# Kernel tuning notes

Measured on AMD Instinct MI355X. Metric: run time of the kernel, lower is better.

## Reference

```python
import jax, jax.numpy as jnp
import numpy as np

V, E, H, T, B = 33278, 400, 1150, 128, 32
LAYER_DIMS = [(E, H), (H, H), (H, E)]  # (input, hidden) per layer; last tied -> E


def _uniform(key, shape, scale):
    return jax.random.uniform(key, shape, jnp.float32, -scale, scale)


def setup_inputs() -> dict:
    key = jax.random.key(0)
    ks = jax.random.split(key, 20)
    inp = {
        'input': jax.random.randint(ks[0], (T, B), 0, V),
        'emb_W': _uniform(ks[1], (V, E), 0.1),
        'final_b': jnp.zeros((V,), jnp.float32),
    }
    ki = 2
    for l, (din, dh) in enumerate(LAYER_DIMS):
        s = 1.0 / np.sqrt(dh)
        inp[f'Wih_l{l}'] = _uniform(ks[ki + 0], (4 * dh, din), s)
        inp[f'Whh_l{l}'] = _uniform(ks[ki + 1], (4 * dh, dh), s)
        inp[f'bih_l{l}'] = _uniform(ks[ki + 2], (4 * dh,), s)
        inp[f'bhh_l{l}'] = _uniform(ks[ki + 3], (4 * dh,), s)
        ki += 4
        inp[f'h0_l{l}'] = jnp.zeros((B, dh), jnp.float32)
        inp[f'c0_l{l}'] = jnp.zeros((B, dh), jnp.float32)
    return inp


def lstm_layer(x, h0, c0, Wih, Whh, bih, bhh):
    # x: [T, B, din]; PyTorch gate order i, f, g, o
    xg = jnp.einsum('tbi,gi->tbg', x, Wih) + bih  # [T, B, 4H]

    def step(carry, xg_t):
        h, c = carry
        g = xg_t + h @ Whh.T + bhh
        i, f, gg, o = jnp.split(g, 4, axis=-1)
        c = jax.nn.sigmoid(f) * c + jax.nn.sigmoid(i) * jnp.tanh(gg)
        h = jax.nn.sigmoid(o) * jnp.tanh(c)
        return (h, c), h

    (hT, cT), ys = jax.lax.scan(step, (h0, c0), xg)
    return ys, hT, cT


def reference(input, emb_W, final_b,
              Wih_l0, Whh_l0, bih_l0, bhh_l0,
              Wih_l1, Whh_l1, bih_l1, bhh_l1,
              Wih_l2, Whh_l2, bih_l2, bhh_l2,
              h0_l0, c0_l0, h0_l1, c0_l1, h0_l2, c0_l2):
    # Eval-mode AWD-LSTM encoder: all dropouts are identity.
    x = emb_W[input]  # [T, B, E]
    params = [(Wih_l0, Whh_l0, bih_l0, bhh_l0, h0_l0, c0_l0),
              (Wih_l1, Whh_l1, bih_l1, bhh_l1, h0_l1, c0_l1),
              (Wih_l2, Whh_l2, bih_l2, bhh_l2, h0_l2, c0_l2)]
    new_hidden = []
    for (Wih, Whh, bih, bhh, h0, c0) in params:
        x, hT, cT = lstm_layer(x, h0, c0, Wih, Whh, bih, bhh)
        new_hidden.extend([hT, cT])
    # Tied decoder: final.weight = embedding.weight ([V, E])
    logits = jnp.einsum('tbe,ve->tbv', x, emb_W) + final_b  # [T, B, V]
    return (logits, *new_hidden)
```

## Files before the change

### kernel.cpp

```cpp
#include <hip/hip_runtime.h>
#include <math.h>

#define T_ 128
#define B_ 32
#define V_ 33278
#define E_ 400

typedef __bf16 bf16x8 __attribute__((ext_vector_type(8)));
typedef float f32x4 __attribute__((ext_vector_type(4)));

#define AGENT_LD(p) __hip_atomic_load((p), __ATOMIC_RELAXED, __HIP_MEMORY_SCOPE_AGENT)
#define AGENT_ST(p, v) __hip_atomic_store((p), (v), __ATOMIC_RELAXED, __HIP_MEMORY_SCOPE_AGENT)

__device__ __forceinline__ float exp2f_(float x) {
  float r;
  asm("v_exp_f32 %0, %1" : "=v"(r) : "v"(x));
  return r;
}
__device__ __forceinline__ float rcpf_(float x) {
  float r;
  asm("v_rcp_f32 %0, %1" : "=v"(r) : "v"(x));
  return r;
}
__device__ __forceinline__ float sigf_(float x) { return rcpf_(1.0f + exp2f_(-1.44269504f * x)); }
__device__ __forceinline__ float tanhf_(float x) {
  float t = exp2f_(2.88539008f * x);
  return 1.0f - 2.0f * rcpf_(t + 1.0f);
}

__device__ __forceinline__ unsigned short f2bf(float f) {
  unsigned u = __float_as_uint(f);
  unsigned lsb = (u >> 16) & 1;
  return (unsigned short)((u + 0x7FFFu + lsb) >> 16);
}

__device__ __forceinline__ void gload16(const unsigned short* g, unsigned short* l) {
  __builtin_amdgcn_global_load_lds((const __attribute__((address_space(1))) void*)g,
                                   (__attribute__((address_space(3))) void*)l, 16, 0, 0);
}

__global__ void embed_kernel(const int* __restrict__ idx, const float* __restrict__ W,
                             unsigned short* __restrict__ x) {
  int i = blockIdx.x * blockDim.x + threadIdx.x;
  if (i >= T_ * B_ * 416) return;
  int k = i % 416;
  int tb = i / 416;
  x[i] = (k < E_) ? f2bf(W[(size_t)idx[tb] * E_ + k]) : 0;
}

__global__ void convW(const float* __restrict__ in, unsigned short* __restrict__ out, int N, int K,
                      int Kp, long total) {
  long i = (long)blockIdx.x * blockDim.x + threadIdx.x;
  if (i >= total) return;
  int k = (int)(i % Kp);
  long n = i / Kp;
  out[i] = (n < N && k < K) ? f2bf(in[n * (long)K + k]) : 0;
}

__global__ __launch_bounds__(256) void gemm_bf16(const unsigned short* __restrict__ A,
                                                 const unsigned short* __restrict__ B,
                                                 const float* __restrict__ bias0,
                                                 const float* __restrict__ bias1,
                                                 float* __restrict__ C, int M, int Kp, int ldc,
                                                 int realN, int gateN) {
  __shared__ __align__(16) unsigned short lsA[4 * 128 * 8];
  __shared__ __align__(16) unsigned short lsB[4 * 128 * 8];
  const int tid = threadIdx.x;
  const int lane = tid & 63;
  const int w = tid >> 6;
  const int wm = (w >> 1) * 64;
  const int wn = (w & 1) * 64;
  const int lr = lane & 15;
  const int kq = lane >> 4;
  const int m0 = blockIdx.y * 128;
  const int n0 = blockIdx.x * 128;

  f32x4 acc[4][4] = {};

  const int kiters = Kp >> 5;
  for (int kt = 0; kt < kiters; ++kt) {
    const int k0 = kt << 5;
#pragma unroll
    for (int q = 0; q < 2; ++q) {
      int s = w + q * 4;
      int kc = s >> 1, rb = (s & 1) * 64;
      gload16(A + (size_t)(m0 + rb + lane) * Kp + k0 + kc * 8, lsA + s * 512);
      gload16(B + (size_t)(n0 + rb + lane) * Kp + k0 + kc * 8, lsB + s * 512);
    }
    __syncthreads();

    bf16x8 af[4], bf[4];
#pragma unroll
    for (int mf = 0; mf < 4; ++mf)
      af[mf] = *(const bf16x8*)&lsA[(kq * 128 + wm + mf * 16 + lr) * 8];
#pragma unroll
    for (int nf = 0; nf < 4; ++nf)
      bf[nf] = *(const bf16x8*)&lsB[(kq * 128 + wn + nf * 16 + lr) * 8];
#pragma unroll
    for (int mf = 0; mf < 4; ++mf)
#pragma unroll
      for (int nf = 0; nf < 4; ++nf)
        acc[mf][nf] = __builtin_amdgcn_mfma_f32_16x16x32_bf16(af[mf], bf[nf], acc[mf][nf], 0, 0, 0);
    __syncthreads();
  }

#pragma unroll
  for (int nf = 0; nf < 4; ++nf) {
    int n = n0 + wn + nf * 16 + lr;
    if (n >= realN) continue;
    float bsum = 0.0f;
    if (bias0) bsum += bias0[n];
    if (bias1) bsum += bias1[n];
    int col = n;
    if (gateN > 0) {
      int g = (n >= gateN) + (n >= 2 * gateN) + (n >= 3 * gateN);
      int u = n - g * gateN;
      col = u * 4 + g;
    }
#pragma unroll
    for (int mf = 0; mf < 4; ++mf) {
      int mbase = m0 + wm + mf * 16 + kq * 4;
#pragma unroll
      for (int r = 0; r < 4; ++r) C[(size_t)(mbase + r) * ldc + col] = acc[mf][nf][r] + bsum;
    }
  }
}


struct FP {
  float* xg;
  const unsigned short *whh0, *wih1, *whh1, *wih2, *whh2;
  const float *h0_0, *c0_0, *h0_1, *c0_1, *h0_2, *c0_2;
  const float *bih1, *bhh1, *bih2, *bhh2;
  unsigned short *xc1, *xc2, *xc3;
  float *oh0, *oc0, *oh1, *oc1, *oh2, *oc2;
  int* flags;
};

__device__ __forceinline__ void pollset(const int* f, int hf, int n, int tgt) {
  int lane = threadIdx.x & 63;
  for (;;) {
    int v = (lane < n) ? AGENT_LD(&f[((lane << 1) + hf) * 16]) : tgt;
    if (__all(v >= tgt)) break;
  }
}

__device__ __forceinline__ void pollone(const int* f, int tgt) {
  for (;;) {
    int v = AGENT_LD(f);
    if (__all(v >= tgt)) break;
  }
}

template <int KT>
__device__ __forceinline__ void stage(const unsigned short* slab, unsigned short* lds) {
  constexpr int KP = KT * 32, KPP = KP + 8, C16 = KP / 8, NCH = 16 * C16;
  constexpr int NIT = (NCH + 511) / 512;
  const int tid = threadIdx.x;
  uint4 d[NIT];
#pragma unroll
  for (int i = 0; i < NIT; ++i) {
    int c = tid + i * 512;
    if (c < NCH) d[i] = *(const uint4*)(slab + (size_t)(c / C16) * KP + (c % C16) * 8);
  }
#pragma unroll
  for (int i = 0; i < NIT; ++i) {
    int c = tid + i * 512;
    if (c < NCH) *(uint4*)&lds[(c / C16) * KPP + (c % C16) * 8] = d[i];
  }
}

template <int KTA, int KTB>
__device__ __forceinline__ void stage2(const unsigned short* slabA, const unsigned short* slabB,
                                       unsigned short* ldsA, unsigned short* ldsB) {
  constexpr int KPA = KTA * 32, KPPA = KPA + 8, CA = KPA / 8, NA = 16 * CA;
  constexpr int NITA = (NA + 511) / 512;
  constexpr int KPB = KTB * 32, KPPB = KPB + 8, CB = KPB / 8, NB = 16 * CB;
  constexpr int NITB = (NB + 511) / 512;
  const int tid = threadIdx.x;
  uint4 dA[NITA], dB[NITB];
#pragma unroll
  for (int i = 0; i < NITA; ++i) {
    int c = tid + i * 512;
    if (c < NA) dA[i] = *(const uint4*)(slabA + (size_t)(c / CA) * KPA + (c % CA) * 8);
  }
#pragma unroll
  for (int i = 0; i < NITB; ++i) {
    int c = tid + i * 512;
    if (c < NB) dB[i] = *(const uint4*)(slabB + (size_t)(c / CB) * KPB + (c % CB) * 8);
  }
#pragma unroll
  for (int i = 0; i < NITA; ++i) {
    int c = tid + i * 512;
    if (c < NA) *(uint4*)&ldsA[(c / CA) * KPPA + (c % CA) * 8] = dA[i];
  }
#pragma unroll
  for (int i = 0; i < NITB; ++i) {
    int c = tid + i * 512;
    if (c < NB) *(uint4*)&ldsB[(c / CB) * KPPB + (c % CB) * 8] = dB[i];
  }
}

template <int KT>
__device__ __forceinline__ void load_aw(const unsigned short* w, int dh, int U0, int wv, int lm,
                                        int kq, bf16x8* aw) {
  const int ga = lm & 3, ula = lm >> 2;
  const int ua = U0 + wv * 4 + ula;
  const unsigned short* wr = w + (size_t)(ga * dh + (ua < dh ? ua : 0)) * (KT * 32);
#pragma unroll
  for (int kt = 0; kt < KT; ++kt) aw[kt] = *(const bf16x8*)&wr[kt * 32 + kq * 8];
}

template <int KT>
__device__ __forceinline__ void mm4(const bf16x8* aw, const unsigned short* lds, int lm, int kq,
                                    f32x4& a0, f32x4& a1, f32x4& a2, f32x4& a3) {
  constexpr int KPP = KT * 32 + 8;
  const unsigned short* rp = lds + lm * KPP + kq * 8;
#pragma unroll
  for (int kt = 0; kt < KT; kt += 4) {
    a0 = __builtin_amdgcn_mfma_f32_16x16x32_bf16(aw[kt], *(const bf16x8*)&rp[kt * 32], a0, 0, 0, 0);
    if (kt + 1 < KT)
      a1 = __builtin_amdgcn_mfma_f32_16x16x32_bf16(aw[kt + 1], *(const bf16x8*)&rp[(kt + 1) * 32],
                                                   a1, 0, 0, 0);
    if (kt + 2 < KT)
      a2 = __builtin_amdgcn_mfma_f32_16x16x32_bf16(aw[kt + 2], *(const bf16x8*)&rp[(kt + 2) * 32],
                                                   a2, 0, 0, 0);
    if (kt + 3 < KT)
      a3 = __builtin_amdgcn_mfma_f32_16x16x32_bf16(aw[kt + 3], *(const bf16x8*)&rp[(kt + 3) * 32],
                                                   a3, 0, 0, 0);
  }
}

__device__ __forceinline__ void pub_h(unsigned short* dst, float hn, bool vu, int kq) {
  unsigned hv = vu ? (unsigned)f2bf(hn) : 0u;
  unsigned t16 = (unsigned)__shfl_xor((int)hv, 16);
  unsigned v32 = (kq & 1) ? (t16 | (hv << 16)) : (hv | (t16 << 16));
  unsigned o32 = (unsigned)__shfl_xor((int)v32, 32);
  if (kq == 0)
    AGENT_ST((unsigned long long*)dst, (unsigned long long)v32 | ((unsigned long long)o32 << 32));
}

__global__ __launch_bounds__(512, 2) void fused_lstm(FP P) {
  __shared__ __align__(16) unsigned short sbuf[16 * 1160 + 16 * 424];
  const int tid = threadIdx.x;
  const int lane = tid & 63;
  const int wv = tid >> 6;
  const int lm = lane & 15;
  const int kq = lane >> 4;
  const int bid = blockIdx.x;
  int* f0 = P.flags;
  int* fh = P.flags + 72 * 16;
  int* f1 = P.flags + 144 * 16;
  int* f2 = P.flags + 216 * 16;
  int* agg = P.flags + 4096;

  if (bid >= 242) {
    if (wv != 0) return;
    const int aset = bid - 242;
    const int hf = aset & 1;
    const int* fset = (aset < 2) ? f0 : f1;
    int* aline = &agg[aset * 16];
    for (int k = 1; k <= T_ + 1; ++k) {
      for (;;) {
        int v = (lane < 36) ? AGENT_LD(&fset[((lane << 1) + hf) * 16]) : k;
        if (__all(v >= k)) break;
      }
      if (lane == 0) AGENT_ST(aline, k);
    }
    return;
  }

  if (bid < 72) {
    constexpr int KT = 36, KP = 1152;
    const int hf = bid & 1, gid = bid >> 1, U0 = gid * 32;
    const int gb = hf * 16 + lm, un = U0 + wv * 4 + kq;
    const bool vu = un < 1150;
    bf16x8 aw[KT];
    load_aw<KT>(P.whh0, 1150, U0, wv, lm, kq, aw);
    float creg = vu ? P.c0_0[gb * 1150 + un] : 0.f;
    pub_h(P.xc1 + (size_t)gb * KP + U0 + wv * 4, vu ? P.h0_0[gb * 1150 + un] : 0.f, vu, kq);
    asm volatile("s_waitcnt vmcnt(0)" ::: "memory");
    __syncthreads();
    if (tid == 0) AGENT_ST(&f0[(gid * 2 + hf) * 16], 1);
    for (int t = 0; t < T_; ++t) {
      f32x4 cinit = *(const f32x4*)&P.xg[(size_t)(t * 32 + gb) * 4608 + un * 4];
      if (wv == 0) pollone(&agg[hf * 16], t + 1);
      __syncthreads();
      stage<KT>(P.xc1 + (size_t)(t * 32 + hf * 16) * KP, sbuf);
      __syncthreads();
      f32x4 a0 = cinit, a1 = {0.f, 0.f, 0.f, 0.f}, a2 = {0.f, 0.f, 0.f, 0.f},
            a3 = {0.f, 0.f, 0.f, 0.f};
      mm4<KT>(aw, sbuf, lm, kq, a0, a1, a2, a3);
      float gi = a0[0] + a1[0] + a2[0] + a3[0], gf = a0[1] + a1[1] + a2[1] + a3[1];
      float gg = a0[2] + a1[2] + a2[2] + a3[2], go = a0[3] + a1[3] + a2[3] + a3[3];
      float cn = sigf_(gf) * creg + sigf_(gi) * tanhf_(gg);
      float hn = sigf_(go) * tanhf_(cn);
      creg = cn;
      pub_h(P.xc1 + (size_t)((t + 1) * 32 + gb) * KP + U0 + wv * 4, hn, vu, kq);
      if (t == T_ - 1 && vu) { P.oh0[gb * 1150 + un] = hn; P.oc0[gb * 1150 + un] = cn; }
      asm volatile("s_waitcnt vmcnt(0)" ::: "memory");
      __syncthreads();
      if (tid == 0) AGENT_ST(&f0[(gid * 2 + hf) * 16], t + 2);
    }
  } else if (bid < 144) {
    constexpr int KT = 36, KP = 1152;
    const int idx = bid - 72, hf = idx & 1, gid = idx >> 1, U0 = gid * 32;
    const int gb = hf * 16 + lm, un = U0 + wv * 4 + kq;
    const bool vu = un < 1150;
    bf16x8 aw[KT];
    load_aw<KT>(P.wih1, 1150, U0, wv, lm, kq, aw);
    f32x4 bini = {0.f, 0.f, 0.f, 0.f};
    if (vu) {
#pragma unroll
      for (int g = 0; g < 4; ++g) bini[g] = P.bih1[g * 1150 + un] + P.bhh1[g * 1150 + un];
    }
    for (int t = 0; t < T_; ++t) {
      if (wv == 0) pollone(&agg[hf * 16], t + 2);
      __syncthreads();
      stage<KT>(P.xc1 + (size_t)((t + 1) * 32 + hf * 16) * KP, sbuf);
      __syncthreads();
      f32x4 a0 = bini, a1 = {0.f, 0.f, 0.f, 0.f}, a2 = {0.f, 0.f, 0.f, 0.f},
            a3 = {0.f, 0.f, 0.f, 0.f};
      mm4<KT>(aw, sbuf, lm, kq, a0, a1, a2, a3);
      float r0 = a0[0] + a1[0] + a2[0] + a3[0], r1 = a0[1] + a1[1] + a2[1] + a3[1];
      float r2 = a0[2] + a1[2] + a2[2] + a3[2], r3 = a0[3] + a1[3] + a2[3] + a3[3];
      unsigned long long* dst =
          (unsigned long long*)(P.xg + (size_t)(t * 32 + gb) * 4608 + un * 4);
      AGENT_ST(dst, ((unsigned long long)__float_as_uint(r1) << 32) | __float_as_uint(r0));
      AGENT_ST(dst + 1, ((unsigned long long)__float_as_uint(r3) << 32) | __float_as_uint(r2));
      asm volatile("s_waitcnt vmcnt(0)" ::: "memory");
      __syncthreads();
      if (tid == 0) AGENT_ST(&fh[(gid * 2 + hf) * 16], t + 1);
    }
  } else if (bid < 216) {
    constexpr int KT = 36, KP = 1152;
    const int idx = bid - 144, hf = idx & 1, gid = idx >> 1, U0 = gid * 32;
    const int gb = hf * 16 + lm, un = U0 + wv * 4 + kq;
    const bool vu = un < 1150;
    bf16x8 aw[KT];
    load_aw<KT>(P.whh1, 1150, U0, wv, lm, kq, aw);
    float creg = vu ? P.c0_1[gb * 1150 + un] : 0.f;
    pub_h(P.xc2 + (size_t)gb * KP + U0 + wv * 4, vu ? P.h0_1[gb * 1150 + un] : 0.f, vu, kq);
    asm volatile("s_waitcnt vmcnt(0)" ::: "memory");
    __syncthreads();
    if (tid == 0) AGENT_ST(&f1[(gid * 2 + hf) * 16], 1);
    for (int t = 0; t < T_; ++t) {
      if (wv == 0) pollone(&agg[32 + hf * 16], t + 1);
      else if (wv == 1) pollone(&fh[(gid * 2 + hf) * 16], t + 1);
      __syncthreads();
      stage<KT>(P.xc2 + (size_t)(t * 32 + hf * 16) * KP, sbuf);
      const unsigned long long* rp =
          (const unsigned long long*)(P.xg + (size_t)(t * 32 + gb) * 4608 + un * 4);
      unsigned long long q0 = AGENT_LD(rp), q1 = AGENT_LD(rp + 1);
      __syncthreads();
      f32x4 a0, a1 = {0.f, 0.f, 0.f, 0.f}, a2 = {0.f, 0.f, 0.f, 0.f}, a3 = {0.f, 0.f, 0.f, 0.f};
      a0[0] = __uint_as_float((unsigned)q0);
      a0[1] = __uint_as_float((unsigned)(q0 >> 32));
      a0[2] = __uint_as_float((unsigned)q1);
      a0[3] = __uint_as_float((unsigned)(q1 >> 32));
      mm4<KT>(aw, sbuf, lm, kq, a0, a1, a2, a3);
      float gi = a0[0] + a1[0] + a2[0] + a3[0], gf = a0[1] + a1[1] + a2[1] + a3[1];
      float gg = a0[2] + a1[2] + a2[2] + a3[2], go = a0[3] + a1[3] + a2[3] + a3[3];
      float cn = sigf_(gf) * creg + sigf_(gi) * tanhf_(gg);
      float hn = sigf_(go) * tanhf_(cn);
      creg = cn;
      pub_h(P.xc2 + (size_t)((t + 1) * 32 + gb) * KP + U0 + wv * 4, hn, vu, kq);
      if (t == T_ - 1 && vu) { P.oh1[gb * 1150 + un] = hn; P.oc1[gb * 1150 + un] = cn; }
      asm volatile("s_waitcnt vmcnt(0)" ::: "memory");
      __syncthreads();
      if (tid == 0) AGENT_ST(&f1[(gid * 2 + hf) * 16], t + 2);
    }
  } else {
    constexpr int KTA = 36, KPA = 1152, KTB = 13, KPB = 416;
    const int idx = bid - 216, hf = idx & 1, gid = idx >> 1, U0 = gid * 32;
    const int gb = hf * 16 + lm, un = U0 + wv * 4 + kq;
    const bool vu = un < 400;
    bf16x8 awi[KTA];
    load_aw<KTA>(P.wih2, 400, U0, wv, lm, kq, awi);
    bf16x8 awh[KTB];
    load_aw<KTB>(P.whh2, 400, U0, wv, lm, kq, awh);
    f32x4 bini = {0.f, 0.f, 0.f, 0.f};
    if (vu) {
#pragma unroll
      for (int g = 0; g < 4; ++g) bini[g] = P.bih2[g * 400 + un] + P.bhh2[g * 400 + un];
    }
    float creg = vu ? P.c0_2[gb * 400 + un] : 0.f;
    pub_h(P.xc3 + (size_t)gb * KPB + U0 + wv * 4, vu ? P.h0_2[gb * 400 + un] : 0.f, vu, kq);
    asm volatile("s_waitcnt vmcnt(0)" ::: "memory");
    __syncthreads();
    if (tid == 0) AGENT_ST(&f2[(gid * 2 + hf) * 16], 1);
    unsigned short* h1buf = sbuf;
    unsigned short* h2buf = sbuf + 16 * (KPA + 8);
    for (int t = 0; t < T_; ++t) {
      if (wv == 0) pollone(&agg[32 + hf * 16], t + 2);
      else if (wv == 1) pollset(f2, hf, 13, t + 1);
      __syncthreads();
      stage2<KTA, KTB>(P.xc2 + (size_t)((t + 1) * 32 + hf * 16) * KPA,
                       P.xc3 + (size_t)(t * 32 + hf * 16) * KPB, h1buf, h2buf);
      __syncthreads();
      f32x4 a0 = bini, a1 = {0.f, 0.f, 0.f, 0.f}, a2 = {0.f, 0.f, 0.f, 0.f},
            a3 = {0.f, 0.f, 0.f, 0.f};
      mm4<KTA>(awi, h1buf, lm, kq, a0, a1, a2, a3);
      mm4<KTB>(awh, h2buf, lm, kq, a0, a1, a2, a3);
      float gi = a0[0] + a1[0] + a2[0] + a3[0], gf = a0[1] + a1[1] + a2[1] + a3[1];
      float gg = a0[2] + a1[2] + a2[2] + a3[2], go = a0[3] + a1[3] + a2[3] + a3[3];
      float cn = sigf_(gf) * creg + sigf_(gi) * tanhf_(gg);
      float hn = sigf_(go) * tanhf_(cn);
      creg = cn;
      pub_h(P.xc3 + (size_t)((t + 1) * 32 + gb) * KPB + U0 + wv * 4, hn, vu, kq);
      if (t == T_ - 1 && vu) { P.oh2[gb * 400 + un] = hn; P.oc2[gb * 400 + un] = cn; }
      asm volatile("s_waitcnt vmcnt(0)" ::: "memory");
      __syncthreads();
      if (tid == 0) AGENT_ST(&f2[(gid * 2 + hf) * 16], t + 2);
    }
  }
}

extern "C" void kernel_launch(void* const* d_in, const int* in_sizes, int n_in, void* d_out,
                              int out_size, void* d_ws, size_t ws_size, hipStream_t stream) {
  const int* input = (const int*)d_in[0];
  const float* emb_W = (const float*)d_in[1];
  const float* final_b = (const float*)d_in[2];

  struct L {
    const float *Wih, *Whh, *bih, *bhh, *h0, *c0;
  };
  L ls[3];
  ls[0] = {(const float*)d_in[3],  (const float*)d_in[4],  (const float*)d_in[5],
           (const float*)d_in[6],  (const float*)d_in[7],  (const float*)d_in[8]};
  ls[1] = {(const float*)d_in[9],  (const float*)d_in[10], (const float*)d_in[11],
           (const float*)d_in[12], (const float*)d_in[13], (const float*)d_in[14]};
  ls[2] = {(const float*)d_in[15], (const float*)d_in[16], (const float*)d_in[17],
           (const float*)d_in[18], (const float*)d_in[19], (const float*)d_in[20]};

  char* base = (char*)d_ws;
  int* flags = (int*)base;
  float* xg0 = (float*)(base + 65536);
  unsigned short* embbf = (unsigned short*)(xg0 + (size_t)4096 * 4608);
  unsigned short* w0 = embbf + (size_t)33280 * 416;
  unsigned short* wih1 = w0 + (size_t)4608 * 416;
  unsigned short* whh0 = wih1 + (size_t)4608 * 1152;
  unsigned short* whh1 = whh0 + (size_t)4600 * 1152;
  unsigned short* wih2 = whh1 + (size_t)4600 * 1152;
  unsigned short* whh2 = wih2 + (size_t)1600 * 1152;
  unsigned short* xemb = whh2 + (size_t)1600 * 416;
  unsigned short* xc1 = xemb + (size_t)4096 * 416;
  unsigned short* xc2 = xc1 + (size_t)4128 * 1152;
  unsigned short* xc3 = xc2 + (size_t)4128 * 1152;
  float* out = (float*)d_out;

  hipMemsetAsync(flags, 0, 65536, stream);

  {
    long tot = (long)33280 * 416;
    convW<<<(unsigned)((tot + 255) / 256), 256, 0, stream>>>(emb_W, embbf, V_, E_, 416, tot);
  }
  {
    long tot = (long)4608 * 416;
    convW<<<(unsigned)((tot + 255) / 256), 256, 0, stream>>>(ls[0].Wih, w0, 4600, 400, 416, tot);
  }
  {
    long tot = (long)4608 * 1152;
    convW<<<(unsigned)((tot + 255) / 256), 256, 0, stream>>>(ls[1].Wih, wih1, 4600, 1150, 1152,
                                                             tot);
  }
  {
    long tot = (long)4600 * 1152;
    convW<<<(unsigned)((tot + 255) / 256), 256, 0, stream>>>(ls[0].Whh, whh0, 4600, 1150, 1152,
                                                             tot);
    convW<<<(unsigned)((tot + 255) / 256), 256, 0, stream>>>(ls[1].Whh, whh1, 4600, 1150, 1152,
                                                             tot);
  }
  {
    long tot = (long)1600 * 1152;
    convW<<<(unsigned)((tot + 255) / 256), 256, 0, stream>>>(ls[2].Wih, wih2, 1600, 1150, 1152,
                                                             tot);
  }
  {
    long tot = (long)1600 * 416;
    convW<<<(unsigned)((tot + 255) / 256), 256, 0, stream>>>(ls[2].Whh, whh2, 1600, 400, 416, tot);
  }
  embed_kernel<<<(T_ * B_ * 416 + 255) / 256, 256, 0, stream>>>(input, emb_W, xemb);

  long o = (long)T_ * B_ * V_;
  float* oh0 = out + o;
  float* oc0 = oh0 + 32 * 1150;
  float* oh1 = oc0 + 32 * 1150;
  float* oc1 = oh1 + 32 * 1150;
  float* oh2 = oc1 + 32 * 1150;
  float* oc2 = oh2 + 32 * 400;

  gemm_bf16<<<dim3(36, 32), 256, 0, stream>>>(xemb, w0, ls[0].bih, ls[0].bhh, xg0, 4096, 416, 4608,
                                              4600, 1150);

  FP P;
  P.xg = xg0;
  P.whh0 = whh0;
  P.wih1 = wih1;
  P.whh1 = whh1;
  P.wih2 = wih2;
  P.whh2 = whh2;
  P.h0_0 = ls[0].h0;
  P.c0_0 = ls[0].c0;
  P.h0_1 = ls[1].h0;
  P.c0_1 = ls[1].c0;
  P.h0_2 = ls[2].h0;
  P.c0_2 = ls[2].c0;
  P.bih1 = ls[1].bih;
  P.bhh1 = ls[1].bhh;
  P.bih2 = ls[2].bih;
  P.bhh2 = ls[2].bhh;
  P.xc1 = xc1;
  P.xc2 = xc2;
  P.xc3 = xc3;
  P.oh0 = oh0;
  P.oc0 = oc0;
  P.oh1 = oh1;
  P.oc1 = oc1;
  P.oh2 = oh2;
  P.oc2 = oc2;
  P.flags = flags;
  fused_lstm<<<246, 512, 0, stream>>>(P);

  gemm_bf16<<<dim3(260, 32), 256, 0, stream>>>(xc3 + (size_t)32 * 416, embbf, final_b, nullptr,
                                               out, 4096, 416, V_, V_, 0);
}
```

Before: 1.518 ms.

## Fuse tied decoder GEMM into persistent LSTM kernel and drop weight conversions

The separate decoder GEMM launch is replaced by an atomic work queue at the end of the persistent LSTM kernel. Each block grabs 128x256 output tiles once the layer-2 flags show the needed timesteps are done, so decoding can overlap the tail of the recurrence. The recurrent kernels now read fp32 weights and convert them to bf16 in registers at load time, which removes five separate conversion kernels. The kernel's occupancy hint drops from 2 to 1 blocks per CU. Risks: the decoder runs on only 246 blocks instead of a large grid, and the wih2 register fill is done twice, first with a wrong row stride and then correctly.

```diff
diff --git a/kernel.cpp b/kernel.cpp
--- a/kernel.cpp
+++ b/kernel.cpp
@@ -5,6 +5,7 @@
 #define B_ 32
 #define V_ 33278
 #define E_ 400
+#define NTILES (32 * 130)
 
 typedef __bf16 bf16x8 __attribute__((ext_vector_type(8)));
 typedef float f32x4 __attribute__((ext_vector_type(4)));
@@ -129,25 +130,28 @@
 
 struct FP {
   float* xg;
-  const unsigned short *whh0, *wih1, *whh1, *wih2, *whh2;
+  const float *whh0, *wih1, *whh1, *wih2, *whh2;
   const float *h0_0, *c0_0, *h0_1, *c0_1, *h0_2, *c0_2;
   const float *bih1, *bhh1, *bih2, *bhh2;
   unsigned short *xc1, *xc2, *xc3;
   float *oh0, *oc0, *oh1, *oc1, *oh2, *oc2;
+  const unsigned short* embbf;
+  const float* fb;
+  float* outp;
   int* flags;
 };
-
-__device__ __forceinline__ void pollset(const int* f, int hf, int n, int tgt) {
-  int lane = threadIdx.x & 63;
-  for (;;) {
-    int v = (lane < n) ? AGENT_LD(&f[((lane << 1) + hf) * 16]) : tgt;
-    if (__all(v >= tgt)) break;
-  }
-}
 
 __device__ __forceinline__ void pollone(const int* f, int tgt) {
   for (;;) {
     int v = AGENT_LD(f);
+    if (__all(v >= tgt)) break;
+  }
+}
+
+__device__ __forceinline__ void pollidx(const int* f, int n, int tgt) {
+  int lane = threadIdx.x & 63;
+  for (;;) {
+    int v = (lane < n) ? AGENT_LD(&f[lane * 16]) : tgt;
     if (__all(v >= tgt)) break;
   }
 }
@@ -202,13 +206,22 @@
 }
 
 template <int KT>
-__device__ __forceinline__ void load_aw(const unsigned short* w, int dh, int U0, int wv, int lm,
-                                        int kq, bf16x8* aw) {
+__device__ __forceinline__ void load_aw(const float* w, int dh, int U0, int wv, int lm, int kq,
+                                        bf16x8* aw) {
   const int ga = lm & 3, ula = lm >> 2;
   const int ua = U0 + wv * 4 + ula;
-  const unsigned short* wr = w + (size_t)(ga * dh + (ua < dh ? ua : 0)) * (KT * 32);
-#pragma unroll
-  for (int kt = 0; kt < KT; ++kt) aw[kt] = *(const bf16x8*)&wr[kt * 32 + kq * 8];
+  const bool va = ua < dh;
+  const float* wr = w + (size_t)(ga * dh + (va ? ua : 0)) * dh;
+#pragma unroll
+  for (int kt = 0; kt < KT; ++kt) {
+    unsigned short tmp[8];
+#pragma unroll
+    for (int j = 0; j < 8; ++j) {
+      int k = kt * 32 + kq * 8 + j;
+      tmp[j] = (va && k < dh) ? f2bf(wr[k]) : (unsigned short)0;
+    }
+    aw[kt] = *(const bf16x8*)tmp;
+  }
 }
 
 template <int KT>
@@ -240,7 +253,75 @@
     AGENT_ST((unsigned long long*)dst, (unsigned long long)v32 | ((unsigned long long)o32 << 32));
 }
 
-__global__ __launch_bounds__(512, 2) void fused_lstm(FP P) {
+__device__ void decoder_queue(const FP& P, unsigned short* sbuf) {
+  __shared__ int qs;
+  const int tid = threadIdx.x;
+  const int lane = tid & 63;
+  const int wv = tid >> 6;
+  const int lr = lane & 15;
+  const int kq = lane >> 4;
+  const int wm = (wv >> 2) * 64;
+  const int wn = (wv & 3) * 64;
+  unsigned short* lsA = sbuf;
+  unsigned short* lsB = sbuf + 4096;
+  int* cnt = P.flags + 8192;
+  int* f2 = P.flags + 216 * 16;
+
+  for (;;) {
+    if (tid == 0) qs = atomicAdd(cnt, 1);
+    __syncthreads();
+    int q = qs;
+    if (q >= NTILES) break;
+    int mt = q / 130, nt = q % 130;
+    if (wv == 0) pollidx(f2, 26, 4 * mt + 5);
+    __syncthreads();
+
+    f32x4 acc[4][4] = {};
+#pragma unroll 1
+    for (int kt = 0; kt < 13; ++kt) {
+      const int k0 = kt << 5;
+      {
+        int s = wv, kc = s >> 1, rb = (s & 1) * 64;
+        gload16(P.xc3 + (size_t)(32 + mt * 128 + rb + lane) * 416 + k0 + kc * 8, lsA + s * 512);
+      }
+#pragma unroll
+      for (int qq = 0; qq < 2; ++qq) {
+        int s = wv + qq * 8, kc = s >> 2, rb = (s & 3) * 64;
+        gload16(P.embbf + (size_t)(nt * 256 + rb + lane) * 416 + k0 + kc * 8, lsB + s * 512);
+      }
+      __syncthreads();
+      bf16x8 af[4], bfv[4];
+#pragma unroll
+      for (int mf = 0; mf < 4; ++mf)
+        af[mf] = *(const bf16x8*)&lsA[(kq * 128 + wm + mf * 16 + lr) * 8];
+#pragma unroll
+      for (int nf = 0; nf < 4; ++nf)
+        bfv[nf] = *(const bf16x8*)&lsB[(kq * 256 + wn + nf * 16 + lr) * 8];
+#pragma unroll
+      for (int mf = 0; mf < 4; ++mf)
+#pragma unroll
+        for (int nf = 0; nf < 4; ++nf)
+          acc[mf][nf] =
+              __builtin_amdgcn_mfma_f32_16x16x32_bf16(af[mf], bfv[nf], acc[mf][nf], 0, 0, 0);
+      __syncthreads();
+    }
+#pragma unroll
+    for (int nf = 0; nf < 4; ++nf) {
+      int n = nt * 256 + wn + nf * 16 + lr;
+      if (n >= V_) continue;
+      float bsum = P.fb[n];
+#pragma unroll
+      for (int mf = 0; mf < 4; ++mf) {
+        int mbase = mt * 128 + wm + mf * 16 + kq * 4;
+#pragma unroll
+        for (int r = 0; r < 4; ++r)
+          P.outp[(size_t)(mbase + r) * V_ + n] = acc[mf][nf][r] + bsum;
+      }
+    }
+  }
+}
+
+__global__ __launch_bounds__(512, 1) void fused_lstm(FP P) {
   __shared__ __align__(16) unsigned short sbuf[16 * 1160 + 16 * 424];
   const int tid = threadIdx.x;
   const int lane = tid & 63;
@@ -377,6 +458,22 @@
     const bool vu = un < 400;
     bf16x8 awi[KTA];
     load_aw<KTA>(P.wih2, 400, U0, wv, lm, kq, awi);
+    {
+      const int ga = lm & 3, ula = lm >> 2;
+      const int ua = U0 + wv * 4 + ula;
+      const bool va = ua < 400;
+      const float* wr = P.wih2 + (size_t)(ga * 400 + (va ? ua : 0)) * 1150;
+#pragma unroll
+      for (int kt = 0; kt < KTA; ++kt) {
+        unsigned short tmp[8];
+#pragma unroll
+        for (int j = 0; j < 8; ++j) {
+          int k = kt * 32 + kq * 8 + j;
+          tmp[j] = (va && k < 1150) ? f2bf(wr[k]) : (unsigned short)0;
+        }
+        awi[kt] = *(const bf16x8*)tmp;
+      }
+    }
     bf16x8 awh[KTB];
     load_aw<KTB>(P.whh2, 400, U0, wv, lm, kq, awh);
     f32x4 bini = {0.f, 0.f, 0.f, 0.f};
@@ -393,7 +490,7 @@
     unsigned short* h2buf = sbuf + 16 * (KPA + 8);
     for (int t = 0; t < T_; ++t) {
       if (wv == 0) pollone(&agg[32 + hf * 16], t + 2);
-      else if (wv == 1) pollset(f2, hf, 13, t + 1);
+      else if (wv == 1) pollidx(f2, 26, t + 1);
       __syncthreads();
       stage2<KTA, KTB>(P.xc2 + (size_t)((t + 1) * 32 + hf * 16) * KPA,
                        P.xc3 + (size_t)(t * 32 + hf * 16) * KPB, h1buf, h2buf);
@@ -414,6 +511,9 @@
       if (tid == 0) AGENT_ST(&f2[(gid * 2 + hf) * 16], t + 2);
     }
   }
+
+  __syncthreads();
+  decoder_queue(P, sbuf);
 }
 
 extern "C" void kernel_launch(void* const* d_in, const int* in_sizes, int n_in, void* d_out,
@@ -438,12 +538,7 @@
   float* xg0 = (float*)(base + 65536);
   unsigned short* embbf = (unsigned short*)(xg0 + (size_t)4096 * 4608);
   unsigned short* w0 = embbf + (size_t)33280 * 416;
-  unsigned short* wih1 = w0 + (size_t)4608 * 416;
-  unsigned short* whh0 = wih1 + (size_t)4608 * 1152;
-  unsigned short* whh1 = whh0 + (size_t)4600 * 1152;
-  unsigned short* wih2 = whh1 + (size_t)4600 * 1152;
-  unsigned short* whh2 = wih2 + (size_t)1600 * 1152;
-  unsigned short* xemb = whh2 + (size_t)1600 * 416;
+  unsigned short* xemb = w0 + (size_t)4608 * 416;
   unsigned short* xc1 = xemb + (size_t)4096 * 416;
   unsigned short* xc2 = xc1 + (size_t)4128 * 1152;
   unsigned short* xc3 = xc2 + (size_t)4128 * 1152;
@@ -458,27 +553,6 @@
   {
     long tot = (long)4608 * 416;
     convW<<<(unsigned)((tot + 255) / 256), 256, 0, stream>>>(ls[0].Wih, w0, 4600, 400, 416, tot);
-  }
-  {
-    long tot = (long)4608 * 1152;
-    convW<<<(unsigned)((tot + 255) / 256), 256, 0, stream>>>(ls[1].Wih, wih1, 4600, 1150, 1152,
-                                                             tot);
-  }
-  {
-    long tot = (long)4600 * 1152;
-    convW<<<(unsigned)((tot + 255) / 256), 256, 0, stream>>>(ls[0].Whh, whh0, 4600, 1150, 1152,
-                                                             tot);
-    convW<<<(unsigned)((tot + 255) / 256), 256, 0, stream>>>(ls[1].Whh, whh1, 4600, 1150, 1152,
-                                                             tot);
-  }
-  {
-    long tot = (long)1600 * 1152;
-    convW<<<(unsigned)((tot + 255) / 256), 256, 0, stream>>>(ls[2].Wih, wih2, 1600, 1150, 1152,
-                                                             tot);
-  }
-  {
-    long tot = (long)1600 * 416;
-    convW<<<(unsigned)((tot + 255) / 256), 256, 0, stream>>>(ls[2].Whh, whh2, 1600, 400, 416, tot);
   }
   embed_kernel<<<(T_ * B_ * 416 + 255) / 256, 256, 0, stream>>>(input, emb_W, xemb);
 
@@ -495,11 +569,11 @@
 
   FP P;
   P.xg = xg0;
-  P.whh0 = whh0;
-  P.wih1 = wih1;
-  P.whh1 = whh1;
-  P.wih2 = wih2;
-  P.whh2 = whh2;
+  P.whh0 = ls[0].Whh;
+  P.wih1 = ls[1].Wih;
+  P.whh1 = ls[1].Whh;
+  P.wih2 = ls[2].Wih;
+  P.whh2 = ls[2].Whh;
   P.h0_0 = ls[0].h0;
   P.c0_0 = ls[0].c0;
   P.h0_1 = ls[1].h0;
@@ -519,9 +593,9 @@
   P.oc1 = oc1;
   P.oh2 = oh2;
   P.oc2 = oc2;
+  P.embbf = embbf;
+  P.fb = final_b;
+  P.outp = out;
   P.flags = flags;
   fused_lstm<<<246, 512, 0, stream>>>(P);
-
-  gemm_bf16<<<dim3(260, 32), 256, 0, stream>>>(xc3 + (size_t)32 * 416, embbf, final_b, nullptr,
-                                               out, 4096, 416, V_, V_, 0);
-}
+}
```

Measured after the change: 1.657 ms. +9.2%, slower.
